# Kernel optimization log

Hardware: AMD Instinct MI355X
Metric: run time of the kernel (lower is better)

## Reference

```python
import jax, jax.numpy as jnp
import numpy as np

T, D, H, E, K = 8192, 2048, 7168, 8, 2


def setup_inputs() -> dict:
    key = jax.random.key(0)
    ks = jax.random.split(key, 5)
    s = 0.02
    return {
        "x": jax.random.normal(ks[0], (T, D), jnp.float32),
        "gate_w": jax.random.normal(ks[1], (E, D), jnp.float32) * s,
        "w1": jax.random.normal(ks[2], (E, H, D), jnp.float32) * s,
        "w2": jax.random.normal(ks[3], (E, H, D), jnp.float32) * s,
        "w3": jax.random.normal(ks[4], (E, H, D), jnp.float32) * s,
    }


def reference(x, gate_w, w1, w2, w3):
    # gate logits [T, E]
    logits = x @ gate_w.T
    vals, idx = jax.lax.top_k(logits, K)                      # [T, K]
    w = jax.nn.softmax(vals.astype(jnp.float32), axis=-1).astype(x.dtype)
    # per-token routing weight for each expert (0 if not selected) [T, E]
    tok = jnp.arange(x.shape[0])
    expert_w = jnp.zeros((x.shape[0], E), x.dtype).at[tok[:, None], idx].add(w)

    # scan over experts: dense SwiGLU per expert, weighted accumulate
    def body(acc, ws):
        w1e, w2e, w3e, we = ws  # [H,D],[H,D],[H,D],[T]
        y = (jax.nn.silu(x @ w1e.T) * (x @ w3e.T)) @ w2e      # [T, D]
        return acc + we[:, None] * y, None

    res, _ = jax.lax.scan(body, jnp.zeros_like(x), (w1, w2, w3, expert_w.T))
    return res
```

## Files before the change

### kernel.cpp

```cpp
#include <hip/hip_runtime.h>

#define TT   8192
#define DDIM 2048
#define HDIM 7168
#define NEXP 8
#define NY1  (HDIM / 128)
#define NY2  (DDIM / 128)
#define NXB  (TT / 128)

typedef __attribute__((ext_vector_type(8))) short bf16x8;
typedef __attribute__((ext_vector_type(4))) short short4v;
typedef __attribute__((ext_vector_type(4))) float f32x4;

__device__ __forceinline__ unsigned short f2bf(float f) {
  unsigned int u = __builtin_bit_cast(unsigned int, f);
  u += 0x7fffu + ((u >> 16) & 1u);
  return (unsigned short)(u >> 16);
}

__device__ __forceinline__ void gload_lds16(const void* gp, void* lp) {
  __builtin_amdgcn_global_load_lds((__attribute__((address_space(1))) void*)gp,
                                   (__attribute__((address_space(3))) void*)lp,
                                   16, 0, 0);
}

__device__ __forceinline__ void mfma16(f32x4& c, bf16x8 a, bf16x8 b) {
  asm("v_mfma_f32_16x16x32_bf16 %0, %1, %2, %0" : "+v"(c) : "v"(a), "v"(b));
}

__global__ __launch_bounds__(256) void cvt_bf16_kernel(const float* __restrict__ src,
                                                       unsigned short* __restrict__ dst,
                                                       long n4) {
  long i = (long)blockIdx.x * 256 + threadIdx.x;
  long stride = (long)gridDim.x * 256;
  for (; i < n4; i += stride) {
    float4 v = ((const float4*)src)[i];
    short4v s;
    s[0] = (short)f2bf(v.x); s[1] = (short)f2bf(v.y);
    s[2] = (short)f2bf(v.z); s[3] = (short)f2bf(v.w);
    ((short4v*)dst)[i] = s;
  }
}

__global__ __launch_bounds__(256) void gate_kernel(const float* __restrict__ x,
                                                   const float* __restrict__ gw,
                                                   int* __restrict__ route_e,
                                                   float* __restrict__ route_w,
                                                   int* __restrict__ counts) {
  int t = blockIdx.x;
  int tid = threadIdx.x;
  const float* xr = x + (size_t)t * DDIM;
  float p[NEXP];
#pragma unroll
  for (int e = 0; e < NEXP; ++e) p[e] = 0.f;
#pragma unroll
  for (int c = 0; c < DDIM / (256 * 4); ++c) {
    int d = (c * 256 + tid) * 4;
    float4 xv = *(const float4*)(xr + d);
#pragma unroll
    for (int e = 0; e < NEXP; ++e) {
      float4 wv = *(const float4*)(gw + (size_t)e * DDIM + d);
      p[e] += xv.x * wv.x + xv.y * wv.y + xv.z * wv.z + xv.w * wv.w;
    }
  }
  __shared__ float red[NEXP][4];
  int lane = tid & 63, wid = tid >> 6;
#pragma unroll
  for (int e = 0; e < NEXP; ++e) {
    float v = p[e];
    for (int o = 32; o > 0; o >>= 1) v += __shfl_down(v, o);
    if (lane == 0) red[e][wid] = v;
  }
  __syncthreads();
  if (tid == 0) {
    float lg[NEXP];
#pragma unroll
    for (int e = 0; e < NEXP; ++e) lg[e] = red[e][0] + red[e][1] + red[e][2] + red[e][3];
    int i0 = 0;
#pragma unroll
    for (int e = 1; e < NEXP; ++e) if (lg[e] > lg[i0]) i0 = e;
    int i1 = -1;
#pragma unroll
    for (int e = 0; e < NEXP; ++e) {
      if (e == i0) continue;
      if (i1 < 0 || lg[e] > lg[i1]) i1 = e;
    }
    float w0 = 1.f / (1.f + __expf(lg[i1] - lg[i0]));
    float w1 = 1.f - w0;
    route_e[t * 2 + 0] = i0;  route_e[t * 2 + 1] = i1;
    route_w[t * 2 + 0] = w0;  route_w[t * 2 + 1] = w1;
    atomicAdd(&counts[i0], 1);
    atomicAdd(&counts[i1], 1);
  }
}

__global__ void scan_kernel(const int* __restrict__ counts, int* __restrict__ offsets,
                            int* __restrict__ cursor) {
  if (threadIdx.x == 0 && blockIdx.x == 0) {
    int o = 0;
    for (int e = 0; e < NEXP; ++e) { offsets[e] = o; cursor[e] = o; o += counts[e]; }
  }
}

__global__ __launch_bounds__(256) void scatter_kernel(const int* __restrict__ route_e,
                                                      const float* __restrict__ route_w,
                                                      int* __restrict__ cursor,
                                                      int* __restrict__ tok_list,
                                                      float* __restrict__ tok_w) {
  int t = blockIdx.x * 256 + threadIdx.x;
  if (t >= TT) return;
#pragma unroll
  for (int s = 0; s < 2; ++s) {
    int e = route_e[t * 2 + s];
    int p = atomicAdd(&cursor[e], 1);
    tok_list[p] = t;
    tok_w[p] = route_w[t * 2 + s];
  }
}

__global__ __launch_bounds__(256) void transpose_w2_kernel(const float* __restrict__ w2,
                                                           unsigned short* __restrict__ w2t,
                                                           int expert_fixed) {
  int e = expert_fixed >= 0 ? expert_fixed : (int)blockIdx.z;
  const float* src = w2 + (size_t)e * HDIM * DDIM;
  unsigned short* dst = w2t + (expert_fixed >= 0 ? (size_t)0 : (size_t)e * DDIM * HDIM);
  int h0 = blockIdx.x * 64, d0 = blockIdx.y * 64;
  __shared__ __align__(8) unsigned short tile[64 * 66];
  int tid = threadIdx.x;
  int hr = tid >> 2;
#pragma unroll
  for (int j = 0; j < 4; ++j) {
    int f4 = (tid & 3) + j * 4;
    float4 v = *(const float4*)(src + (size_t)(h0 + hr) * DDIM + d0 + f4 * 4);
    unsigned int lo = (unsigned int)f2bf(v.x) | ((unsigned int)f2bf(v.y) << 16);
    unsigned int hi = (unsigned int)f2bf(v.z) | ((unsigned int)f2bf(v.w) << 16);
    char* bp = (char*)tile + hr * 132 + f4 * 8;
    *(unsigned int*)bp = lo;
    *(unsigned int*)(bp + 4) = hi;
  }
  __syncthreads();
  int dr = tid >> 2;
  int hbase = (tid & 3) * 16;
  unsigned short vals[16];
#pragma unroll
  for (int i = 0; i < 16; ++i)
    vals[i] = *(unsigned short*)((char*)tile + (hbase + i) * 132 + dr * 2);
  unsigned short* op = dst + (size_t)(d0 + dr) * HDIM + h0 + hbase;
#pragma unroll
  for (int j = 0; j < 4; ++j) {
    short4v s;
    s[0] = (short)vals[j * 4 + 0]; s[1] = (short)vals[j * 4 + 1];
    s[2] = (short)vals[j * 4 + 2]; s[3] = (short)vals[j * 4 + 3];
    *(short4v*)(op + j * 4) = s;
  }
}

__global__ __launch_bounds__(256, 2) void gemm1_kernel(
    const unsigned short* __restrict__ xbf, const unsigned short* __restrict__ w1b,
    const unsigned short* __restrict__ w3b, const int* __restrict__ tok_list,
    const int* __restrict__ counts, const int* __restrict__ offsets,
    unsigned short* __restrict__ g, int expert_fixed) {
  int nwg = gridDim.x;
  int orig = blockIdx.x;
  int wg = (orig & 7) * (nwg >> 3) + (orig >> 3);
  int nx = wg % NXB;
  int rem = wg / NXB;
  int ny = rem % NY1;
  int e = expert_fixed >= 0 ? expert_fixed : rem / NY1;

  int cnt = counts[e];
  int mbase = nx * 128;
  if (mbase >= cnt) return;
  int off = offsets[e];
  int gshift = expert_fixed >= 0 ? 0 : off;
  int nbase = ny * 128;
  int rows = cnt - mbase; if (rows > 128) rows = 128;

  const unsigned short* w1e = expert_fixed >= 0 ? w1b : w1b + (size_t)e * HDIM * DDIM;
  const unsigned short* w3e = expert_fixed >= 0 ? w3b : w3b + (size_t)e * HDIM * DDIM;

  __shared__ __align__(16) unsigned short As[2][128 * 32];
  __shared__ __align__(16) unsigned short B1s[2][128 * 32];
  __shared__ __align__(16) unsigned short B3s[2][128 * 32];

  int tid = threadIdx.x, lane = tid & 63, wid = tid >> 6;
  int wr = wid >> 1, wc = wid & 1;

  size_t tokoff[2];
  const char* w1p[2]; const char* w3p[2];
#pragma unroll
  for (int t2 = 0; t2 < 2; ++t2) {
    int r = wid * 32 + t2 * 16 + (lane >> 2);
    int m = mbase + r; if (m > cnt - 1) m = cnt - 1;
    int tok = tok_list[off + m];
    tokoff[t2] = (size_t)tok * (DDIM * 2) + (size_t)((lane & 3) * 16);
    int br = nbase + r;
    w1p[t2] = (const char*)w1e + (size_t)br * (DDIM * 2) + (lane & 3) * 16;
    w3p[t2] = (const char*)w3e + (size_t)br * (DDIM * 2) + (lane & 3) * 16;
  }
  const char* xb = (const char*)xbf;

  f32x4 zv = {0.f, 0.f, 0.f, 0.f};
  f32x4 acc1[4][4], acc3[4][4];
#pragma unroll
  for (int mi = 0; mi < 4; ++mi)
#pragma unroll
    for (int ni = 0; ni < 4; ++ni) { acc1[mi][ni] = zv; acc3[mi][ni] = zv; }

  auto stage = [&](int buf, int ks) {
    char* Ad  = (char*)&As[buf][0]  + wid * 2048;
    char* B1d = (char*)&B1s[buf][0] + wid * 2048;
    char* B3d = (char*)&B3s[buf][0] + wid * 2048;
    size_t ko = (size_t)ks * 64;
    gload_lds16(xb + tokoff[0] + ko, Ad);
    gload_lds16(xb + tokoff[1] + ko, Ad + 1024);
    gload_lds16(w1p[0] + ko, B1d);
    gload_lds16(w1p[1] + ko, B1d + 1024);
    gload_lds16(w3p[0] + ko, B3d);
    gload_lds16(w3p[1] + ko, B3d + 1024);
  };

  stage(0, 0);
  __syncthreads();
  for (int ks = 0; ks < DDIM / 32; ++ks) {
    int cur = ks & 1;
    if (ks + 1 < DDIM / 32) stage(cur ^ 1, ks + 1);
    bf16x8 a[4], b1[4], b3[4];
#pragma unroll
    for (int mi = 0; mi < 4; ++mi)
      a[mi] = *(const bf16x8*)&As[cur][(wr * 64 + mi * 16 + (lane & 15)) * 32 + (lane >> 4) * 8];
#pragma unroll
    for (int ni = 0; ni < 4; ++ni) {
      int ro = (wc * 64 + ni * 16 + (lane & 15)) * 32 + (lane >> 4) * 8;
      b1[ni] = *(const bf16x8*)&B1s[cur][ro];
      b3[ni] = *(const bf16x8*)&B3s[cur][ro];
    }
#pragma unroll
    for (int ni = 0; ni < 4; ++ni)
#pragma unroll
      for (int mi = 0; mi < 4; ++mi) {
        mfma16(acc1[mi][ni], a[mi], b1[ni]);
        mfma16(acc3[mi][ni], a[mi], b3[ni]);
      }
    __syncthreads();
  }

#pragma unroll
  for (int mi = 0; mi < 4; ++mi) {
#pragma unroll
    for (int q = 0; q < 4; ++q) {
      int rl = wr * 64 + mi * 16 + (lane >> 4) * 4 + q;
      if (rl >= rows) continue;
      size_t grow = (size_t)(mbase + rl + gshift);
      unsigned short* gp = g + grow * HDIM + nbase + wc * 64 + (lane & 15);
#pragma unroll
      for (int ni = 0; ni < 4; ++ni) {
        float v1 = acc1[mi][ni][q];
        float v3 = acc3[mi][ni][q];
        float gv = (v1 / (1.f + __expf(-v1))) * v3;
        gp[ni * 16] = f2bf(gv);
      }
    }
  }
}

__global__ __launch_bounds__(256, 2) void gemm2_kernel(
    const unsigned short* __restrict__ g, const unsigned short* __restrict__ w2t,
    const int* __restrict__ tok_list, const float* __restrict__ tok_w,
    const int* __restrict__ counts, const int* __restrict__ offsets,
    float* __restrict__ out, int expert_fixed) {
  int nwg = gridDim.x;
  int orig = blockIdx.x;
  int wg = (orig & 7) * (nwg >> 3) + (orig >> 3);
  int nx = wg % NXB;
  int rem = wg / NXB;
  int ny = rem % NY2;
  int e = expert_fixed >= 0 ? expert_fixed : rem / NY2;

  int cnt = counts[e];
  int mbase = nx * 128;
  if (mbase >= cnt) return;
  int off = offsets[e];
  int gshift = expert_fixed >= 0 ? 0 : off;
  int nbase = ny * 128;
  int rows = cnt - mbase; if (rows > 128) rows = 128;
  const unsigned short* w2te = w2t + (expert_fixed >= 0 ? (size_t)0 : (size_t)e * DDIM * HDIM);

  __shared__ __align__(16) unsigned short As[2][128 * 32];
  __shared__ __align__(16) unsigned short Bs[2][128 * 32];

  int tid = threadIdx.x, lane = tid & 63, wid = tid >> 6;
  int wr = wid >> 1, wc = wid & 1;

  size_t aoff[2], boff[2];
#pragma unroll
  for (int t2 = 0; t2 < 2; ++t2) {
    int r = wid * 32 + t2 * 16 + (lane >> 2);
    int m = mbase + r; if (m > cnt - 1) m = cnt - 1;
    aoff[t2] = (size_t)(m + gshift) * (HDIM * 2) + (size_t)((lane & 3) * 16);
    boff[t2] = (size_t)(nbase + r) * (HDIM * 2) + (size_t)((lane & 3) * 16);
  }

  f32x4 zv = {0.f, 0.f, 0.f, 0.f};
  f32x4 acc[4][4];
#pragma unroll
  for (int mi = 0; mi < 4; ++mi)
#pragma unroll
    for (int ni = 0; ni < 4; ++ni) acc[mi][ni] = zv;

  const char* gb = (const char*)g;
  const char* wb = (const char*)w2te;

  auto stage = [&](int buf, int ks) {
    char* Ad = (char*)&As[buf][0] + wid * 2048;
    char* Bd = (char*)&Bs[buf][0] + wid * 2048;
    size_t ko = (size_t)ks * 64;
    gload_lds16(gb + aoff[0] + ko, Ad);
    gload_lds16(gb + aoff[1] + ko, Ad + 1024);
    gload_lds16(wb + boff[0] + ko, Bd);
    gload_lds16(wb + boff[1] + ko, Bd + 1024);
  };

  stage(0, 0);
  __syncthreads();
  for (int ks = 0; ks < HDIM / 32; ++ks) {
    int cur = ks & 1;
    if (ks + 1 < HDIM / 32) stage(cur ^ 1, ks + 1);
    bf16x8 a[4], b[4];
#pragma unroll
    for (int mi = 0; mi < 4; ++mi)
      a[mi] = *(const bf16x8*)&As[cur][(wr * 64 + mi * 16 + (lane & 15)) * 32 + (lane >> 4) * 8];
#pragma unroll
    for (int ni = 0; ni < 4; ++ni)
      b[ni] = *(const bf16x8*)&Bs[cur][(wc * 64 + ni * 16 + (lane & 15)) * 32 + (lane >> 4) * 8];
#pragma unroll
    for (int ni = 0; ni < 4; ++ni)
#pragma unroll
      for (int mi = 0; mi < 4; ++mi) mfma16(acc[mi][ni], a[mi], b[ni]);
    __syncthreads();
  }
#pragma unroll
  for (int mi = 0; mi < 4; ++mi) {
#pragma unroll
    for (int q = 0; q < 4; ++q) {
      int rl = wr * 64 + mi * 16 + (lane >> 4) * 4 + q;
      if (rl >= rows) continue;
      int m = mbase + rl;
      int tok = tok_list[off + m];
      float wt = tok_w[off + m];
      float* op = out + (size_t)tok * DDIM + nbase + wc * 64 + (lane & 15);
#pragma unroll
      for (int ni = 0; ni < 4; ++ni)
        atomicAdd(op + ni * 16, acc[mi][ni][q] * wt);
    }
  }
}

extern "C" void kernel_launch(void* const* d_in, const int* in_sizes, int n_in,
                              void* d_out, int out_size, void* d_ws, size_t ws_size,
                              hipStream_t stream) {
  const float* x      = (const float*)d_in[0];
  const float* gate_w = (const float*)d_in[1];
  const float* w1     = (const float*)d_in[2];
  const float* w2     = (const float*)d_in[3];
  const float* w3     = (const float*)d_in[4];
  float* out = (float*)d_out;
  char* ws = (char*)d_ws;

  size_t o = 0;
  int* counts  = (int*)(ws + o);
  int* offsets = counts + 8;
  int* cursor  = counts + 16;
  o += 256;
  int*   route_e = (int*)(ws + o);   o += (size_t)TT * 2 * 4;
  float* route_w = (float*)(ws + o); o += (size_t)TT * 2 * 4;
  int*   tok_list = (int*)(ws + o);  o += (size_t)TT * 2 * 4;
  float* tok_w = (float*)(ws + o);   o += (size_t)TT * 2 * 4;
  unsigned short* xbf = (unsigned short*)(ws + o); o += (size_t)TT * DDIM * 2;
  size_t fixed = o;

  const size_t WSZ = (size_t)HDIM * DDIM;
  const size_t wbf_full = (size_t)NEXP * WSZ * 2;
  const size_t gfull = (size_t)TT * 2 * HDIM * 2;

  hipMemsetAsync(counts, 0, 8 * sizeof(int), stream);
  hipMemsetAsync(out, 0, (size_t)TT * DDIM * sizeof(float), stream);
  cvt_bf16_kernel<<<4096, 256, 0, stream>>>(x, xbf, (long)TT * DDIM / 4);
  gate_kernel<<<TT, 256, 0, stream>>>(x, gate_w, route_e, route_w, counts);
  scan_kernel<<<1, 64, 0, stream>>>(counts, offsets, cursor);
  scatter_kernel<<<(TT + 255) / 256, 256, 0, stream>>>(route_e, route_w, cursor, tok_list, tok_w);

  if (ws_size >= fixed + 3 * wbf_full + gfull) {
    unsigned short* w1b = (unsigned short*)(ws + fixed);
    unsigned short* w3b = w1b + NEXP * WSZ;
    unsigned short* w2t = w3b + NEXP * WSZ;
    unsigned short* gbuf = w2t + NEXP * WSZ;
    cvt_bf16_kernel<<<8192, 256, 0, stream>>>(w1, w1b, (long)(NEXP * WSZ / 4));
    cvt_bf16_kernel<<<8192, 256, 0, stream>>>(w3, w3b, (long)(NEXP * WSZ / 4));
    transpose_w2_kernel<<<dim3(HDIM / 64, DDIM / 64, NEXP), 256, 0, stream>>>(w2, w2t, -1);
    gemm1_kernel<<<NXB * NY1 * NEXP, 256, 0, stream>>>(
        xbf, w1b, w3b, tok_list, counts, offsets, gbuf, -1);
    gemm2_kernel<<<NXB * NY2 * NEXP, 256, 0, stream>>>(
        gbuf, w2t, tok_list, tok_w, counts, offsets, out, -1);
  } else {
    unsigned short* w1b = (unsigned short*)(ws + fixed);
    unsigned short* w3b = w1b + WSZ;
    unsigned short* w2t = w3b + WSZ;
    unsigned short* gbuf = w2t + WSZ;
    for (int e = 0; e < NEXP; ++e) {
      cvt_bf16_kernel<<<4096, 256, 0, stream>>>(w1 + (size_t)e * WSZ, w1b, (long)(WSZ / 4));
      cvt_bf16_kernel<<<4096, 256, 0, stream>>>(w3 + (size_t)e * WSZ, w3b, (long)(WSZ / 4));
      transpose_w2_kernel<<<dim3(HDIM / 64, DDIM / 64, 1), 256, 0, stream>>>(w2, w2t, e);
      gemm1_kernel<<<NXB * NY1, 256, 0, stream>>>(
          xbf, w1b, w3b, tok_list, counts, offsets, gbuf, e);
      gemm2_kernel<<<NXB * NY2, 256, 0, stream>>>(
          gbuf, w2t, tok_list, tok_w, counts, offsets, out, e);
    }
  }
}
```

Before: 2.693 ms.

## Enlarge GEMM tiles to 256x256 with 512 threads, swizzled LDS, and deeper K step

Both expert GEMMs move from 128x128 tiles with 256 threads to 256x256 tiles with 512 threads and 64-wide K steps. In gemm1 the w1 and w3 rows are packed into one 256-wide B tile, and the SwiGLU combine goes through an LDS exchange between wave groups. The LDS layout gets an XOR swizzle to avoid bank conflicts, and s_setprio is raised around the MFMA bursts. The larger tiles give more operand reuse per byte loaded, at the cost of about 128KB of LDS per block, which at launch_bounds(512,2) may limit occupancy to one block per CU.

Result: slower. 2.772 ms (+3.0%).

```diff
diff --git a/kernel.cpp b/kernel.cpp
--- a/kernel.cpp
+++ b/kernel.cpp
@@ -4,9 +4,9 @@
 #define DDIM 2048
 #define HDIM 7168
 #define NEXP 8
-#define NY1  (HDIM / 128)
-#define NY2  (DDIM / 128)
-#define NXB  (TT / 128)
+#define MT   32
+#define NT1  (HDIM / 128)
+#define NT2  (DDIM / 256)
 
 typedef __attribute__((ext_vector_type(8))) short bf16x8;
 typedef __attribute__((ext_vector_type(4))) short short4v;
@@ -155,205 +155,241 @@
   }
 }
 
-__global__ __launch_bounds__(256, 2) void gemm1_kernel(
+
+__global__ __launch_bounds__(512, 2) void gemm1_kernel(
     const unsigned short* __restrict__ xbf, const unsigned short* __restrict__ w1b,
     const unsigned short* __restrict__ w3b, const int* __restrict__ tok_list,
     const int* __restrict__ counts, const int* __restrict__ offsets,
     unsigned short* __restrict__ g, int expert_fixed) {
+  __shared__ __align__(16) char smem[133120];
+  constexpr int NK = DDIM / 64;
+
   int nwg = gridDim.x;
   int orig = blockIdx.x;
   int wg = (orig & 7) * (nwg >> 3) + (orig >> 3);
-  int nx = wg % NXB;
-  int rem = wg / NXB;
-  int ny = rem % NY1;
-  int e = expert_fixed >= 0 ? expert_fixed : rem / NY1;
+  int mt = wg & (MT - 1);
+  int rem = wg >> 5;
+  int nt = rem % NT1;
+  int e = expert_fixed >= 0 ? expert_fixed : rem / NT1;
 
   int cnt = counts[e];
-  int mbase = nx * 128;
+  int mbase = mt * 256;
   if (mbase >= cnt) return;
   int off = offsets[e];
   int gshift = expert_fixed >= 0 ? 0 : off;
-  int nbase = ny * 128;
-  int rows = cnt - mbase; if (rows > 128) rows = 128;
+  int rows = cnt - mbase; if (rows > 256) rows = 256;
 
   const unsigned short* w1e = expert_fixed >= 0 ? w1b : w1b + (size_t)e * HDIM * DDIM;
   const unsigned short* w3e = expert_fixed >= 0 ? w3b : w3b + (size_t)e * HDIM * DDIM;
 
-  __shared__ __align__(16) unsigned short As[2][128 * 32];
-  __shared__ __align__(16) unsigned short B1s[2][128 * 32];
-  __shared__ __align__(16) unsigned short B3s[2][128 * 32];
-
   int tid = threadIdx.x, lane = tid & 63, wid = tid >> 6;
-  int wr = wid >> 1, wc = wid & 1;
-
-  size_t tokoff[2];
-  const char* w1p[2]; const char* w3p[2];
-#pragma unroll
-  for (int t2 = 0; t2 < 2; ++t2) {
-    int r = wid * 32 + t2 * 16 + (lane >> 2);
+  int wr = wid >> 2, wc = wid & 3;
+
+  int r16 = lane >> 2;
+  int csrc = (lane & 3) ^ ((lane >> 3) & 3);
+  const char* asrc[2]; const char* bsrc[2];
+#pragma unroll
+  for (int j = 0; j < 2; ++j) {
+    int r = wid * 32 + j * 16 + r16;
     int m = mbase + r; if (m > cnt - 1) m = cnt - 1;
     int tok = tok_list[off + m];
-    tokoff[t2] = (size_t)tok * (DDIM * 2) + (size_t)((lane & 3) * 16);
-    int br = nbase + r;
-    w1p[t2] = (const char*)w1e + (size_t)br * (DDIM * 2) + (lane & 3) * 16;
-    w3p[t2] = (const char*)w3e + (size_t)br * (DDIM * 2) + (lane & 3) * 16;
-  }
-  const char* xb = (const char*)xbf;
+    asrc[j] = (const char*)xbf + (size_t)tok * (DDIM * 2) + csrc * 16;
+    const char* base = (r < 128)
+        ? (const char*)w1e + (size_t)(nt * 128 + r) * (DDIM * 2)
+        : (const char*)w3e + (size_t)(nt * 128 + r - 128) * (DDIM * 2);
+    bsrc[j] = base + csrc * 16;
+  }
+  int rowA = (wr * 128 + (lane & 15)) * 64;
+  int rowB = (wc * 64  + (lane & 15)) * 64;
+  int ckr  = (((lane >> 4) ^ ((lane >> 1) & 3)) * 16);
 
   f32x4 zv = {0.f, 0.f, 0.f, 0.f};
-  f32x4 acc1[4][4], acc3[4][4];
-#pragma unroll
-  for (int mi = 0; mi < 4; ++mi)
-#pragma unroll
-    for (int ni = 0; ni < 4; ++ni) { acc1[mi][ni] = zv; acc3[mi][ni] = zv; }
-
-  auto stage = [&](int buf, int ks) {
-    char* Ad  = (char*)&As[buf][0]  + wid * 2048;
-    char* B1d = (char*)&B1s[buf][0] + wid * 2048;
-    char* B3d = (char*)&B3s[buf][0] + wid * 2048;
-    size_t ko = (size_t)ks * 64;
-    gload_lds16(xb + tokoff[0] + ko, Ad);
-    gload_lds16(xb + tokoff[1] + ko, Ad + 1024);
-    gload_lds16(w1p[0] + ko, B1d);
-    gload_lds16(w1p[1] + ko, B1d + 1024);
-    gload_lds16(w3p[0] + ko, B3d);
-    gload_lds16(w3p[1] + ko, B3d + 1024);
+  f32x4 acc[8][4];
+#pragma unroll
+  for (int m = 0; m < 8; ++m)
+#pragma unroll
+    for (int n = 0; n < 4; ++n) acc[m][n] = zv;
+
+  auto STAGE = [&](int buf, int kt) {
+    char* base = smem + buf * 65536;
+    size_t ko = (size_t)kt * 128;
+#pragma unroll
+    for (int s = 0; s < 2; ++s)
+#pragma unroll
+      for (int j = 0; j < 2; ++j) {
+        char* dA = base + s * 16384 + wid * 2048 + j * 1024;
+        char* dB = base + 32768 + s * 16384 + wid * 2048 + j * 1024;
+        gload_lds16(asrc[j] + ko + s * 64, dA);
+        gload_lds16(bsrc[j] + ko + s * 64, dB);
+      }
   };
 
-  stage(0, 0);
+  STAGE(0, 0);
   __syncthreads();
-  for (int ks = 0; ks < DDIM / 32; ++ks) {
-    int cur = ks & 1;
-    if (ks + 1 < DDIM / 32) stage(cur ^ 1, ks + 1);
-    bf16x8 a[4], b1[4], b3[4];
-#pragma unroll
-    for (int mi = 0; mi < 4; ++mi)
-      a[mi] = *(const bf16x8*)&As[cur][(wr * 64 + mi * 16 + (lane & 15)) * 32 + (lane >> 4) * 8];
-#pragma unroll
-    for (int ni = 0; ni < 4; ++ni) {
-      int ro = (wc * 64 + ni * 16 + (lane & 15)) * 32 + (lane >> 4) * 8;
-      b1[ni] = *(const bf16x8*)&B1s[cur][ro];
-      b3[ni] = *(const bf16x8*)&B3s[cur][ro];
-    }
-#pragma unroll
-    for (int ni = 0; ni < 4; ++ni)
-#pragma unroll
-      for (int mi = 0; mi < 4; ++mi) {
-        mfma16(acc1[mi][ni], a[mi], b1[ni]);
-        mfma16(acc3[mi][ni], a[mi], b3[ni]);
+  int buf = 0;
+  for (int kt = 0; kt < NK; ++kt) {
+    if (kt + 1 < NK) STAGE(buf ^ 1, kt + 1);
+    char* Ab = smem + buf * 65536;
+    char* Bb = Ab + 32768;
+#pragma unroll
+    for (int ks = 0; ks < 2; ++ks) {
+      bf16x8 af[8], bfr[4];
+#pragma unroll
+      for (int mi = 0; mi < 8; ++mi)
+        af[mi] = *(const bf16x8*)(Ab + ks * 16384 + rowA + mi * 1024 + ckr);
+#pragma unroll
+      for (int ni = 0; ni < 4; ++ni)
+        bfr[ni] = *(const bf16x8*)(Bb + ks * 16384 + rowB + ni * 1024 + ckr);
+      __builtin_amdgcn_s_setprio(1);
+#pragma unroll
+      for (int ni = 0; ni < 4; ++ni)
+#pragma unroll
+        for (int mi = 0; mi < 8; ++mi) mfma16(acc[mi][ni], af[mi], bfr[ni]);
+      __builtin_amdgcn_s_setprio(0);
+    }
+    __syncthreads();
+    buf ^= 1;
+  }
+
+  float* hb = (float*)smem;
+  if (wc < 2) {
+#pragma unroll
+    for (int m = 0; m < 8; ++m)
+#pragma unroll
+      for (int q = 0; q < 4; ++q) {
+        int row = wr * 128 + m * 16 + (lane >> 4) * 4 + q;
+        int col = wc * 64 + (lane & 15);
+#pragma unroll
+        for (int n = 0; n < 4; ++n)
+          hb[row * 130 + col + n * 16] = acc[m][n][q];
       }
-    __syncthreads();
-  }
-
-#pragma unroll
-  for (int mi = 0; mi < 4; ++mi) {
-#pragma unroll
-    for (int q = 0; q < 4; ++q) {
-      int rl = wr * 64 + mi * 16 + (lane >> 4) * 4 + q;
-      if (rl >= rows) continue;
-      size_t grow = (size_t)(mbase + rl + gshift);
-      unsigned short* gp = g + grow * HDIM + nbase + wc * 64 + (lane & 15);
-#pragma unroll
-      for (int ni = 0; ni < 4; ++ni) {
-        float v1 = acc1[mi][ni][q];
-        float v3 = acc3[mi][ni][q];
-        float gv = (v1 / (1.f + __expf(-v1))) * v3;
-        gp[ni * 16] = f2bf(gv);
+  }
+  __syncthreads();
+  if (wc >= 2) {
+#pragma unroll
+    for (int m = 0; m < 8; ++m)
+#pragma unroll
+      for (int q = 0; q < 4; ++q) {
+        int row = wr * 128 + m * 16 + (lane >> 4) * 4 + q;
+        if (row >= rows) continue;
+        size_t grow = (size_t)(mbase + row + gshift);
+        int colbase = (wc - 2) * 64 + (lane & 15);
+        unsigned short* gp = g + grow * HDIM + nt * 128 + colbase;
+#pragma unroll
+        for (int n = 0; n < 4; ++n) {
+          float h1 = hb[row * 130 + colbase + n * 16];
+          float h3 = acc[m][n][q];
+          float gv = (h1 / (1.f + __expf(-h1))) * h3;
+          gp[n * 16] = f2bf(gv);
+        }
       }
-    }
-  }
-}
-
-__global__ __launch_bounds__(256, 2) void gemm2_kernel(
+  }
+}
+
+__global__ __launch_bounds__(512, 2) void gemm2_kernel(
     const unsigned short* __restrict__ g, const unsigned short* __restrict__ w2t,
     const int* __restrict__ tok_list, const float* __restrict__ tok_w,
     const int* __restrict__ counts, const int* __restrict__ offsets,
     float* __restrict__ out, int expert_fixed) {
+  __shared__ __align__(16) char smem[131072];
+  constexpr int NK = HDIM / 64;
+
   int nwg = gridDim.x;
   int orig = blockIdx.x;
   int wg = (orig & 7) * (nwg >> 3) + (orig >> 3);
-  int nx = wg % NXB;
-  int rem = wg / NXB;
-  int ny = rem % NY2;
-  int e = expert_fixed >= 0 ? expert_fixed : rem / NY2;
+  int mt = wg & (MT - 1);
+  int rem = wg >> 5;
+  int nt = rem % NT2;
+  int e = expert_fixed >= 0 ? expert_fixed : rem / NT2;
 
   int cnt = counts[e];
-  int mbase = nx * 128;
+  int mbase = mt * 256;
   if (mbase >= cnt) return;
   int off = offsets[e];
   int gshift = expert_fixed >= 0 ? 0 : off;
-  int nbase = ny * 128;
-  int rows = cnt - mbase; if (rows > 128) rows = 128;
+  int nbase = nt * 256;
+  int rows = cnt - mbase; if (rows > 256) rows = 256;
   const unsigned short* w2te = w2t + (expert_fixed >= 0 ? (size_t)0 : (size_t)e * DDIM * HDIM);
 
-  __shared__ __align__(16) unsigned short As[2][128 * 32];
-  __shared__ __align__(16) unsigned short Bs[2][128 * 32];
-
   int tid = threadIdx.x, lane = tid & 63, wid = tid >> 6;
-  int wr = wid >> 1, wc = wid & 1;
-
-  size_t aoff[2], boff[2];
-#pragma unroll
-  for (int t2 = 0; t2 < 2; ++t2) {
-    int r = wid * 32 + t2 * 16 + (lane >> 2);
+  int wr = wid >> 2, wc = wid & 3;
+
+  int r16 = lane >> 2;
+  int csrc = (lane & 3) ^ ((lane >> 3) & 3);
+  const char* asrc[2]; const char* bsrc[2];
+#pragma unroll
+  for (int j = 0; j < 2; ++j) {
+    int r = wid * 32 + j * 16 + r16;
     int m = mbase + r; if (m > cnt - 1) m = cnt - 1;
-    aoff[t2] = (size_t)(m + gshift) * (HDIM * 2) + (size_t)((lane & 3) * 16);
-    boff[t2] = (size_t)(nbase + r) * (HDIM * 2) + (size_t)((lane & 3) * 16);
-  }
+    asrc[j] = (const char*)g + (size_t)(m + gshift) * (HDIM * 2) + csrc * 16;
+    bsrc[j] = (const char*)w2te + (size_t)(nbase + r) * (HDIM * 2) + csrc * 16;
+  }
+  int rowA = (wr * 128 + (lane & 15)) * 64;
+  int rowB = (wc * 64  + (lane & 15)) * 64;
+  int ckr  = (((lane >> 4) ^ ((lane >> 1) & 3)) * 16);
 
   f32x4 zv = {0.f, 0.f, 0.f, 0.f};
-  f32x4 acc[4][4];
-#pragma unroll
-  for (int mi = 0; mi < 4; ++mi)
-#pragma unroll
-    for (int ni = 0; ni < 4; ++ni) acc[mi][ni] = zv;
-
-  const char* gb = (const char*)g;
-  const char* wb = (const char*)w2te;
-
-  auto stage = [&](int buf, int ks) {
-    char* Ad = (char*)&As[buf][0] + wid * 2048;
-    char* Bd = (char*)&Bs[buf][0] + wid * 2048;
-    size_t ko = (size_t)ks * 64;
-    gload_lds16(gb + aoff[0] + ko, Ad);
-    gload_lds16(gb + aoff[1] + ko, Ad + 1024);
-    gload_lds16(wb + boff[0] + ko, Bd);
-    gload_lds16(wb + boff[1] + ko, Bd + 1024);
+  f32x4 acc[8][4];
+#pragma unroll
+  for (int m = 0; m < 8; ++m)
+#pragma unroll
+    for (int n = 0; n < 4; ++n) acc[m][n] = zv;
+
+  auto STAGE = [&](int buf, int kt) {
+    char* base = smem + buf * 65536;
+    size_t ko = (size_t)kt * 128;
+#pragma unroll
+    for (int s = 0; s < 2; ++s)
+#pragma unroll
+      for (int j = 0; j < 2; ++j) {
+        char* dA = base + s * 16384 + wid * 2048 + j * 1024;
+        char* dB = base + 32768 + s * 16384 + wid * 2048 + j * 1024;
+        gload_lds16(asrc[j] + ko + s * 64, dA);
+        gload_lds16(bsrc[j] + ko + s * 64, dB);
+      }
   };
 
-  stage(0, 0);
+  STAGE(0, 0);
   __syncthreads();
-  for (int ks = 0; ks < HDIM / 32; ++ks) {
-    int cur = ks & 1;
-    if (ks + 1 < HDIM / 32) stage(cur ^ 1, ks + 1);
-    bf16x8 a[4], b[4];
-#pragma unroll
-    for (int mi = 0; mi < 4; ++mi)
-      a[mi] = *(const bf16x8*)&As[cur][(wr * 64 + mi * 16 + (lane & 15)) * 32 + (lane >> 4) * 8];
-#pragma unroll
-    for (int ni = 0; ni < 4; ++ni)
-      b[ni] = *(const bf16x8*)&Bs[cur][(wc * 64 + ni * 16 + (lane & 15)) * 32 + (lane >> 4) * 8];
-#pragma unroll
-    for (int ni = 0; ni < 4; ++ni)
-#pragma unroll
-      for (int mi = 0; mi < 4; ++mi) mfma16(acc[mi][ni], a[mi], b[ni]);
+  int buf = 0;
+  for (int kt = 0; kt < NK; ++kt) {
+    if (kt + 1 < NK) STAGE(buf ^ 1, kt + 1);
+    char* Ab = smem + buf * 65536;
+    char* Bb = Ab + 32768;
+#pragma unroll
+    for (int ks = 0; ks < 2; ++ks) {
+      bf16x8 af[8], bfr[4];
+#pragma unroll
+      for (int mi = 0; mi < 8; ++mi)
+        af[mi] = *(const bf16x8*)(Ab + ks * 16384 + rowA + mi * 1024 + ckr);
+#pragma unroll
+      for (int ni = 0; ni < 4; ++ni)
+        bfr[ni] = *(const bf16x8*)(Bb + ks * 16384 + rowB + ni * 1024 + ckr);
+      __builtin_amdgcn_s_setprio(1);
+#pragma unroll
+      for (int ni = 0; ni < 4; ++ni)
+#pragma unroll
+        for (int mi = 0; mi < 8; ++mi) mfma16(acc[mi][ni], af[mi], bfr[ni]);
+      __builtin_amdgcn_s_setprio(0);
+    }
     __syncthreads();
-  }
-#pragma unroll
-  for (int mi = 0; mi < 4; ++mi) {
+    buf ^= 1;
+  }
+
+#pragma unroll
+  for (int m = 0; m < 8; ++m)
 #pragma unroll
     for (int q = 0; q < 4; ++q) {
-      int rl = wr * 64 + mi * 16 + (lane >> 4) * 4 + q;
-      if (rl >= rows) continue;
-      int m = mbase + rl;
-      int tok = tok_list[off + m];
-      float wt = tok_w[off + m];
+      int row = wr * 128 + m * 16 + (lane >> 4) * 4 + q;
+      if (row >= rows) continue;
+      int mi = mbase + row;
+      int tok = tok_list[off + mi];
+      float wt = tok_w[off + mi];
       float* op = out + (size_t)tok * DDIM + nbase + wc * 64 + (lane & 15);
 #pragma unroll
-      for (int ni = 0; ni < 4; ++ni)
-        atomicAdd(op + ni * 16, acc[mi][ni][q] * wt);
-    }
-  }
+      for (int n = 0; n < 4; ++n)
+        atomicAdd(op + n * 16, acc[m][n][q] * wt);
+    }
 }
 
 extern "C" void kernel_launch(void* const* d_in, const int* in_sizes, int n_in,
@@ -398,9 +434,9 @@
     cvt_bf16_kernel<<<8192, 256, 0, stream>>>(w1, w1b, (long)(NEXP * WSZ / 4));
     cvt_bf16_kernel<<<8192, 256, 0, stream>>>(w3, w3b, (long)(NEXP * WSZ / 4));
     transpose_w2_kernel<<<dim3(HDIM / 64, DDIM / 64, NEXP), 256, 0, stream>>>(w2, w2t, -1);
-    gemm1_kernel<<<NXB * NY1 * NEXP, 256, 0, stream>>>(
+    gemm1_kernel<<<MT * NT1 * NEXP, 512, 0, stream>>>(
         xbf, w1b, w3b, tok_list, counts, offsets, gbuf, -1);
-    gemm2_kernel<<<NXB * NY2 * NEXP, 256, 0, stream>>>(
+    gemm2_kernel<<<MT * NT2 * NEXP, 512, 0, stream>>>(
         gbuf, w2t, tok_list, tok_w, counts, offsets, out, -1);
   } else {
     unsigned short* w1b = (unsigned short*)(ws + fixed);
@@ -411,9 +447,9 @@
       cvt_bf16_kernel<<<4096, 256, 0, stream>>>(w1 + (size_t)e * WSZ, w1b, (long)(WSZ / 4));
       cvt_bf16_kernel<<<4096, 256, 0, stream>>>(w3 + (size_t)e * WSZ, w3b, (long)(WSZ / 4));
       transpose_w2_kernel<<<dim3(HDIM / 64, DDIM / 64, 1), 256, 0, stream>>>(w2, w2t, e);
-      gemm1_kernel<<<NXB * NY1, 256, 0, stream>>>(
+      gemm1_kernel<<<MT * NT1, 512, 0, stream>>>(
           xbf, w1b, w3b, tok_list, counts, offsets, gbuf, e);
-      gemm2_kernel<<<NXB * NY2, 256, 0, stream>>>(
+      gemm2_kernel<<<MT * NT2, 512, 0, stream>>>(
           gbuf, w2t, tok_list, tok_w, counts, offsets, out, e);
     }
   }
```
